# Kernel optimization log

Hardware: AMD Instinct MI355X
Metric: run time of the kernel (lower is better)

## Reference

```python
import jax, jax.numpy as jnp
import numpy as np
from jax import lax

IMAGE_SIZE = (224, 224)
NUM_NN = 3
SIGMA = 4


def _gaussian_kernel1d(sigma: float) -> jnp.ndarray:
    # anomalib/kornia: kernel_size = 2 * int(4.0 * sigma + 0.5) + 1
    ksize = 2 * int(4.0 * sigma + 0.5) + 1
    x = jnp.arange(ksize, dtype=jnp.float32) - ksize // 2
    g = jnp.exp(-(x * x) / (2.0 * sigma * sigma))
    return g / jnp.sum(g)


def _gaussian_blur(x: jnp.ndarray, sigma: float) -> jnp.ndarray:
    # x: [B, 1, H, W]; reflect 'same' padding + separable depthwise conv
    g = _gaussian_kernel1d(sigma)
    k = g.shape[0]
    pad = k // 2
    x = jnp.pad(x, ((0, 0), (0, 0), (pad, pad), (pad, pad)), mode='reflect')
    dn = ('NCHW', 'OIHW', 'NCHW')
    x = lax.conv_general_dilated(x, g.reshape(1, 1, k, 1), (1, 1), 'VALID', dimension_numbers=dn)
    x = lax.conv_general_dilated(x, g.reshape(1, 1, 1, k), (1, 1), 'VALID', dimension_numbers=dn)
    return x


def setup_inputs() -> dict:
    key = jax.random.key(0)
    distance = jax.random.uniform(key, (16, 3136, 4096), dtype=jnp.float32)
    return {"distance": distance, "scale_h": 56, "scale_w": 56}


def reference(distance, scale_h, scale_w):
    b = distance.shape[0]
    d = jnp.sqrt(distance)                                   # [B, HW, M]
    # topk smallest (ascending), like torch.topk(largest=False)
    vals = -lax.top_k(-d, NUM_NN)[0]                         # [B, HW, K]
    w = jax.nn.softmax(-vals, axis=-1)                       # softmin
    s = w[:, :, 0] * vals[:, :, 0]                           # [B, HW]
    score = s.reshape(b, 1, scale_h, scale_w)                # 'b (h w) c -> b c h w', c=1
    score = lax.stop_gradient(score)                         # .detach()
    amap = jnp.mean(score, axis=1, keepdims=True)            # [B, 1, h, w]
    amap = jax.image.resize(amap, (b, 1, IMAGE_SIZE[0], IMAGE_SIZE[1]), method='bilinear')
    return _gaussian_blur(amap, SIGMA)
```

## Files before the change

kernel.cpp:

```cpp
#include <hip/hip_runtime.h>

#define NB   16
#define HW   3136
#define MEL  4096
#define SH   56
#define SW   56
#define OH   224
#define OW   224
#define KRAD 16
#define NPIX (NB * OH * OW)

typedef float vf4 __attribute__((ext_vector_type(4)));

__device__ __forceinline__ void ins3(float v, float& m0, float& m1, float& m2) {
    float a = fminf(v, m0);
    float b = fmaxf(v, m0);
    m0 = a;
    float c = fminf(b, m1);
    float d = fmaxf(b, m1);
    m1 = c;
    m2 = fminf(d, m2);
}

__global__ __launch_bounds__(256) void topk_score_kernel(const float* __restrict__ dist,
                                                         float* __restrict__ score) {
    const int wid  = threadIdx.x >> 6;
    const int lane = threadIdx.x & 63;
    const long long row = (long long)blockIdx.x * 4 + wid;
    const vf4* p = (const vf4*)(dist + row * (long long)MEL);

    vf4 v[16];
    #pragma unroll
    for (int j = 0; j < 16; ++j)
        v[j] = __builtin_nontemporal_load(p + lane + 64 * j);

    float a0 = 3.4e38f, a1 = 3.4e38f, a2 = 3.4e38f;
    float b0 = 3.4e38f, b1 = 3.4e38f, b2 = 3.4e38f;

    #pragma unroll
    for (int j = 0; j < 16; ++j) {
        ins3(v[j][0], a0, a1, a2);
        ins3(v[j][1], b0, b1, b2);
        ins3(v[j][2], a0, a1, a2);
        ins3(v[j][3], b0, b1, b2);
    }
    ins3(b0, a0, a1, a2);
    ins3(b1, a0, a1, a2);
    ins3(b2, a0, a1, a2);

    #pragma unroll
    for (int off = 32; off > 0; off >>= 1) {
        float s0 = __shfl_xor(a0, off);
        float s1 = __shfl_xor(a1, off);
        float s2 = __shfl_xor(a2, off);
        ins3(s0, a0, a1, a2);
        ins3(s1, a0, a1, a2);
        ins3(s2, a0, a1, a2);
    }

    if (lane == 0) {
        float v0 = sqrtf(a0), v1 = sqrtf(a1), v2 = sqrtf(a2);
        score[row] = v0 / (1.0f + expf(v0 - v1) + expf(v0 - v2));
    }
}

__global__ __launch_bounds__(256) void post_kernel(const float* __restrict__ score,
                                                   float* __restrict__ out) {
    __shared__ float g[2 * KRAD + 1];
    __shared__ float row[OW];
    __shared__ float snorm;

    const int tid = threadIdx.x;
    if (tid < 2 * KRAD + 1) {
        float k = (float)(tid - KRAD);
        g[tid] = expf(-k * k * (1.0f / 32.0f));
    }
    __syncthreads();
    if (tid == 0) {
        float s = 0.0f;
        #pragma unroll
        for (int j = 0; j < 2 * KRAD + 1; ++j) s += g[j];
        snorm = 1.0f / (s * s);
    }

    const int b = blockIdx.x / OH;
    const int y = blockIdx.x % OH;
    const float* s = score + b * (SH * SW);
    const int x = tid;

    if (x < OW) {
        float sx = fmaxf((x + 0.5f) * 0.25f - 0.5f, 0.0f);
        int   x0 = (int)sx;
        float fx = sx - (float)x0;
        int   x1 = min(x0 + 1, SW - 1);

        float acc = 0.0f;
        #pragma unroll
        for (int k = -KRAD; k <= KRAD; ++k) {
            int yy = y + k;
            yy = (yy < 0) ? -yy : yy;
            yy = (yy > OH - 1) ? (2 * (OH - 1) - yy) : yy;
            float sy = fmaxf((yy + 0.5f) * 0.25f - 0.5f, 0.0f);
            int   y0 = (int)sy;
            float fy = sy - (float)y0;
            int   y1 = min(y0 + 1, SH - 1);
            const float* r0 = s + y0 * SW;
            const float* r1 = s + y1 * SW;
            float v00 = r0[x0], v01 = r0[x1];
            float v10 = r1[x0], v11 = r1[x1];
            float e0 = v00 + (v01 - v00) * fx;
            float e1 = v10 + (v11 - v10) * fx;
            acc += g[k + KRAD] * (e0 + (e1 - e0) * fy);
        }
        row[x] = acc;
    }
    __syncthreads();

    if (x < OW) {
        float acc = 0.0f;
        #pragma unroll
        for (int k = -KRAD; k <= KRAD; ++k) {
            int xx = x + k;
            xx = (xx < 0) ? -xx : xx;
            xx = (xx > OW - 1) ? (2 * (OW - 1) - xx) : xx;
            acc += g[k + KRAD] * row[xx];
        }
        out[blockIdx.x * OW + x] = acc * snorm;
    }
}

extern "C" void kernel_launch(void* const* d_in, const int* in_sizes, int n_in,
                              void* d_out, int out_size, void* d_ws, size_t ws_size,
                              hipStream_t stream) {
    const float* dist = (const float*)d_in[0];
    float* out = (float*)d_out;
    float* scorebuf = (float*)d_ws;

    topk_score_kernel<<<(NB * HW) / 4, 256, 0, stream>>>(dist, scorebuf);
    post_kernel<<<NB * OH, 256, 0, stream>>>(scorebuf, out);
}
```

Before: 152.9 us.

## Fold bilinear upsample and Gaussian blur into a precomputed banded matrix

Precomputes a 56x224 matrix that combines reflect-padded Gaussian blur with bilinear upsampling, built by a small extra kernel each call. The post kernel then applies it separably with 12-tap banded dot products on the 56x56 score grid instead of 33-tap loops over upsampled coordinates. This cuts arithmetic and gathers in the post stage but adds a kernel launch. The top-k kernel also gets an occupancy hint in its launch bounds. The total is dominated by streaming the roughly 800MB distance tensor, so the post-stage savings are small relative to that.

```diff
diff --git a/kernel.cpp b/kernel.cpp
--- a/kernel.cpp
+++ b/kernel.cpp
@@ -8,7 +8,6 @@
 #define OH   224
 #define OW   224
 #define KRAD 16
-#define NPIX (NB * OH * OW)
 
 typedef float vf4 __attribute__((ext_vector_type(4)));
 
@@ -22,8 +21,8 @@
     m2 = fminf(d, m2);
 }
 
-__global__ __launch_bounds__(256) void topk_score_kernel(const float* __restrict__ dist,
-                                                         float* __restrict__ score) {
+__global__ __launch_bounds__(256, 4) void topk_score_kernel(const float* __restrict__ dist,
+                                                            float* __restrict__ score) {
     const int wid  = threadIdx.x >> 6;
     const int lane = threadIdx.x & 63;
     const long long row = (long long)blockIdx.x * 4 + wid;
@@ -64,68 +63,62 @@
     }
 }
 
+__global__ __launch_bounds__(256) void build_At_kernel(float* __restrict__ At) {
+    int id = blockIdx.x * 256 + threadIdx.x;
+    if (id >= SH * OH) return;
+    int j = id / OH;
+    int y = id % OH;
+
+    float gsum = 0.0f, acc = 0.0f;
+    #pragma unroll
+    for (int k = -KRAD; k <= KRAD; ++k) {
+        float g = expf((float)(-k * k) * (1.0f / 32.0f));
+        gsum += g;
+        int f = y + k;
+        f = (f < 0) ? -f : f;
+        f = (f > OH - 1) ? (2 * (OH - 1) - f) : f;
+        float sy = fmaxf((f + 0.5f) * 0.25f - 0.5f, 0.0f);
+        int   y0 = (int)sy;
+        float fy = sy - (float)y0;
+        int   y1 = min(y0 + 1, SH - 1);
+        float w = ((y0 == j) ? (1.0f - fy) : 0.0f) + ((y1 == j) ? fy : 0.0f);
+        acc += g * w;
+    }
+    At[id] = acc / gsum;
+}
+
 __global__ __launch_bounds__(256) void post_kernel(const float* __restrict__ score,
+                                                   const float* __restrict__ At,
                                                    float* __restrict__ out) {
-    __shared__ float g[2 * KRAD + 1];
-    __shared__ float row[OW];
-    __shared__ float snorm;
-
-    const int tid = threadIdx.x;
-    if (tid < 2 * KRAD + 1) {
-        float k = (float)(tid - KRAD);
-        g[tid] = expf(-k * k * (1.0f / 32.0f));
-    }
-    __syncthreads();
-    if (tid == 0) {
-        float s = 0.0f;
-        #pragma unroll
-        for (int j = 0; j < 2 * KRAD + 1; ++j) s += g[j];
-        snorm = 1.0f / (s * s);
-    }
-
+    __shared__ float tmp[SW];
     const int b = blockIdx.x / OH;
     const int y = blockIdx.x % OH;
+    const int tid = threadIdx.x;
     const float* s = score + b * (SH * SW);
-    const int x = tid;
 
-    if (x < OW) {
-        float sx = fmaxf((x + 0.5f) * 0.25f - 0.5f, 0.0f);
-        int   x0 = (int)sx;
-        float fx = sx - (float)x0;
-        int   x1 = min(x0 + 1, SW - 1);
+    const int wy = min(max((int)floorf((y - 15.5f) * 0.25f - 0.5f), 0), SH - 12);
 
+    if (tid < SW) {
         float acc = 0.0f;
         #pragma unroll
-        for (int k = -KRAD; k <= KRAD; ++k) {
-            int yy = y + k;
-            yy = (yy < 0) ? -yy : yy;
-            yy = (yy > OH - 1) ? (2 * (OH - 1) - yy) : yy;
-            float sy = fmaxf((yy + 0.5f) * 0.25f - 0.5f, 0.0f);
-            int   y0 = (int)sy;
-            float fy = sy - (float)y0;
-            int   y1 = min(y0 + 1, SH - 1);
-            const float* r0 = s + y0 * SW;
-            const float* r1 = s + y1 * SW;
-            float v00 = r0[x0], v01 = r0[x1];
-            float v10 = r1[x0], v11 = r1[x1];
-            float e0 = v00 + (v01 - v00) * fx;
-            float e1 = v10 + (v11 - v10) * fx;
-            acc += g[k + KRAD] * (e0 + (e1 - e0) * fy);
+        for (int t = 0; t < 12; ++t) {
+            int j = wy + t;
+            acc += At[j * OH + y] * s[j * SW + tid];
         }
-        row[x] = acc;
+        tmp[tid] = acc;
     }
     __syncthreads();
 
-    if (x < OW) {
+    if (tid < OW) {
+        const int x = tid;
+        const int wx = min(max((int)floorf((x - 15.5f) * 0.25f - 0.5f), 0), SH - 12);
         float acc = 0.0f;
         #pragma unroll
-        for (int k = -KRAD; k <= KRAD; ++k) {
-            int xx = x + k;
-            xx = (xx < 0) ? -xx : xx;
-            xx = (xx > OW - 1) ? (2 * (OW - 1) - xx) : xx;
-            acc += g[k + KRAD] * row[xx];
+        for (int t = 0; t < 12; ++t) {
+            int j = wx + t;
+            acc += At[j * OH + x] * tmp[j];
         }
-        out[blockIdx.x * OW + x] = acc * snorm;
+        out[blockIdx.x * OW + x] = acc;
     }
 }
 
@@ -134,8 +127,11 @@
                               hipStream_t stream) {
     const float* dist = (const float*)d_in[0];
     float* out = (float*)d_out;
+
     float* scorebuf = (float*)d_ws;
+    float* At       = (float*)((char*)d_ws + 50176 * 4);
 
+    build_At_kernel<<<(SH * OH + 255) / 256, 256, 0, stream>>>(At);
     topk_score_kernel<<<(NB * HW) / 4, 256, 0, stream>>>(dist, scorebuf);
-    post_kernel<<<NB * OH, 256, 0, stream>>>(scorebuf, out);
+    post_kernel<<<NB * OH, 256, 0, stream>>>(scorebuf, At, out);
 }
```

Result: faster. 145.3 us (-5.0%).
